# Optimization experiments

Hardware: AMD Instinct MI355X
Metric: run time of the kernel (lower is better)

## Reference

```python
import jax, jax.numpy as jnp
import numpy as np

NBITS = 8          # attn_nbits
GROUP = 32         # per-group size along head_dim for Q/K quantizers
H = 16             # num_heads
EPS = 1e-8


def _ste(x, q):
    # straight-through estimator: forward=q, backward=identity
    return x + jax.lax.stop_gradient(q - x)


def pg_dynamic_quant(x, group_size=GROUP, nbits=NBITS):
    """Per-group symmetric dynamic fake-quant along last dim (ActPGDynamicQuantizer)."""
    qmax = 2.0 ** (nbits - 1) - 1
    lead, D = x.shape[:-1], x.shape[-1]
    xg = x.reshape(*lead, D // group_size, group_size)
    s = jnp.maximum(jnp.max(jnp.abs(xg), axis=-1, keepdims=True) / qmax, EPS)
    q = jnp.clip(jnp.round(xg / s), -qmax - 1.0, qmax) * s
    return _ste(x, q.reshape(x.shape))


def dynamic_quant(x, axis=2, nbits=NBITS):
    """Symmetric dynamic fake-quant, scale shared along `axis` (ActDynamicQuantizer)."""
    qmax = 2.0 ** (nbits - 1) - 1
    s = jnp.maximum(jnp.max(jnp.abs(x), axis=axis, keepdims=True) / qmax, EPS)
    q = jnp.clip(jnp.round(x / s), -qmax - 1.0, qmax) * s
    return _ste(x, q)


def static_scale_quant(x, nbits=NBITS):
    """Unsigned static-scale fake-quant for softmax map in [0,1] (ActStaticScaleQuantizer)."""
    qmax = 2.0 ** nbits - 1
    q = jnp.clip(jnp.round(x * qmax), 0.0, qmax) / qmax
    return _ste(x, q)


def setup_inputs() -> dict:
    key = jax.random.key(0)
    ks = jax.random.split(key, 7)
    B, L, C = 4, 1024, 1024
    return {
        "x":         jax.random.normal(ks[0], (B, L, C), jnp.float32),
        "attn_bias": jax.random.normal(ks[1], (1, 1, L, L), jnp.float32) * 0.1,
        "w_qkv":     jax.random.normal(ks[2], (3 * C, C), jnp.float32) * 0.02,
        "q_bias":    jax.random.normal(ks[3], (C,), jnp.float32) * 0.02,
        "v_bias":    jax.random.normal(ks[4], (C,), jnp.float32) * 0.02,
        "w_proj":    jax.random.normal(ks[5], (C, C), jnp.float32) * 0.02,
        "b_proj":    jax.random.normal(ks[6], (C,), jnp.float32) * 0.02,
    }


def reference(x, attn_bias, w_qkv, q_bias, v_bias, w_proj, b_proj):
    B, L, C = x.shape
    D = C // H
    scale = D ** -0.5
    # qkv projection: bias-free linear + concat(q_bias, zeros_k, v_bias)
    bias = jnp.concatenate([q_bias, jnp.zeros_like(q_bias), v_bias])
    qkv = (x @ w_qkv.T + bias).reshape(B, L, 3, H, D)
    q, k, v = jnp.transpose(qkv, (2, 0, 3, 1, 4))  # each [B,H,L,D]
    # inline fake-quantization (MODE 0 inference path)
    qq = pg_dynamic_quant(q)
    kk = pg_dynamic_quant(k)
    vv = dynamic_quant(v, axis=2)
    attn = jnp.einsum('bhld,bhmd->bhlm', qq * scale, kk) + attn_bias  # [B,H,L,L]
    a = jax.nn.softmax(attn, axis=-1)
    a = static_scale_quant(a)
    out = jnp.einsum('bhlm,bhmd->bhld', a, vv)
    out = jnp.transpose(out, (0, 2, 1, 3)).reshape(B, L, C)
    return out @ w_proj.T + b_proj
```

## Files before the change

### kernel.cpp

```cpp
#include <hip/hip_runtime.h>


typedef unsigned short u16;
typedef unsigned int u32;
typedef __attribute__((ext_vector_type(8))) _Float16 half8;
typedef __attribute__((ext_vector_type(4))) float f32x4;

__device__ __forceinline__ u16 f2b(float f) {
    u32 i;
    __builtin_memcpy(&i, &f, 4);
    return (u16)((i + 0x7FFFu + ((i >> 16) & 1u)) >> 16);
}

__device__ __forceinline__ void split16(float v, u16& hi, u16& lo) {
    _Float16 h = (_Float16)v;
    _Float16 l = (_Float16)(v - (float)h);
    __builtin_memcpy(&hi, &h, 2);
    __builtin_memcpy(&lo, &l, 2);
}

__device__ __forceinline__ int dot4(int a, int b, int c) {
#if __has_builtin(__builtin_amdgcn_sdot4)
    return __builtin_amdgcn_sdot4(a, b, c, false);
#else
    int r = c;
    r += ((a << 24) >> 24) * ((b << 24) >> 24);
    r += ((a << 16) >> 24) * ((b << 16) >> 24);
    r += ((a << 8) >> 24) * ((b << 8) >> 24);
    r += (a >> 24) * (b >> 24);
    return r;
#endif
}

__global__ __launch_bounds__(256) void cvt_bf16w(u16* __restrict__ dst,
                                                 const float* __restrict__ src, int n) {
    int i = (blockIdx.x * 256 + threadIdx.x) * 4;
    if (i + 3 < n) {
        float4 v = *(const float4*)(src + i);
        ushort4 o;
        o.x = f2b(v.x); o.y = f2b(v.y); o.z = f2b(v.z); o.w = f2b(v.w);
        *(ushort4*)(dst + i) = o;
    }
}

__global__ __launch_bounds__(256) void gemm_qkv3(const float* __restrict__ A,
                                                 const float* __restrict__ Bm,
                                                 const float* __restrict__ qbias,
                                                 const float* __restrict__ vbias,
                                                 float* __restrict__ qws,
                                                 float* __restrict__ kws,
                                                 float* __restrict__ vws) {
    __shared__ u16 Ah[128 * 32], Al[128 * 32], Bh[128 * 32], Bl[128 * 32];
    const int t = threadIdx.x;
    const int lane = t & 63, w = t >> 6;
    const int wm = w >> 1, wn = w & 1;
    const int srow = t >> 2, scol = (t & 3) * 8;
    const int lm = lane & 15, lk = (lane >> 4) * 8;
    const int bm = blockIdx.y, bn = blockIdx.x;

    const float* ap = A + (size_t)(bm * 128 + srow) * 1024 + scol;
    const float* bp = Bm + (size_t)(bn * 128 + srow) * 1024 + scol;

    double dacc[4][4][4];
#pragma unroll
    for (int i = 0; i < 4; i++)
#pragma unroll
        for (int j = 0; j < 4; j++)
#pragma unroll
            for (int r = 0; r < 4; r++) dacc[i][j][r] = 0.0;

    for (int slab = 0; slab < 8; slab++) {
        f32x4 acc[4][4];
#pragma unroll
        for (int i = 0; i < 4; i++)
#pragma unroll
            for (int j = 0; j < 4; j++) acc[i][j] = (f32x4){0.f, 0.f, 0.f, 0.f};

        for (int kc = 0; kc < 4; kc++) {
            const int k0 = slab * 128 + kc * 32;
            float vreg[4][8];
#pragma unroll
            for (int e = 0; e < 4; e++) {
                const float* src = (e < 2) ? (ap + (e & 1) * (size_t)64 * 1024 + k0)
                                           : (bp + (e & 1) * (size_t)64 * 1024 + k0);
                float4 v0 = *(const float4*)(src);
                float4 v1 = *(const float4*)(src + 4);
                vreg[e][0] = v0.x; vreg[e][1] = v0.y; vreg[e][2] = v0.z; vreg[e][3] = v0.w;
                vreg[e][4] = v1.x; vreg[e][5] = v1.y; vreg[e][6] = v1.z; vreg[e][7] = v1.w;
            }
            __syncthreads();
#pragma unroll
            for (int e = 0; e < 4; e++) {
                union { u16 us[8]; uint4 v; } ph, pl;
#pragma unroll
                for (int j = 0; j < 8; j++) split16(vreg[e][j], ph.us[j], pl.us[j]);
                u16* dh = (e < 2) ? Ah : Bh;
                u16* dl = (e < 2) ? Al : Bl;
                int row = srow + (e & 1) * 64;
                *(uint4*)(dh + row * 32 + scol) = ph.v;
                *(uint4*)(dl + row * 32 + scol) = pl.v;
            }
            __syncthreads();

            half8 fah[4], fal[4], fbh[4], fbl[4];
#pragma unroll
            for (int i = 0; i < 4; i++) {
                int ra = (wm * 64 + i * 16 + lm) * 32 + lk;
                int rb = (wn * 64 + i * 16 + lm) * 32 + lk;
                fah[i] = *(const half8*)(Ah + ra);
                fal[i] = *(const half8*)(Al + ra);
                fbh[i] = *(const half8*)(Bh + rb);
                fbl[i] = *(const half8*)(Bl + rb);
            }
#pragma unroll
            for (int mi = 0; mi < 4; mi++)
#pragma unroll
                for (int ni = 0; ni < 4; ni++) {
                    acc[mi][ni] = __builtin_amdgcn_mfma_f32_16x16x32_f16(
                        fal[mi], fbh[ni], acc[mi][ni], 0, 0, 0);
                    acc[mi][ni] = __builtin_amdgcn_mfma_f32_16x16x32_f16(
                        fah[mi], fbl[ni], acc[mi][ni], 0, 0, 0);
                    acc[mi][ni] = __builtin_amdgcn_mfma_f32_16x16x32_f16(
                        fah[mi], fbh[ni], acc[mi][ni], 0, 0, 0);
                }
        }
#pragma unroll
        for (int i = 0; i < 4; i++)
#pragma unroll
            for (int j = 0; j < 4; j++)
#pragma unroll
                for (int r = 0; r < 4; r++) dacc[i][j][r] += (double)acc[i][j][r];
    }

    const int rbase = bm * 128 + wm * 64 + (lane >> 4) * 4;
    const int cbase = bn * 128 + wn * 64 + lm;
#pragma unroll
    for (int mi = 0; mi < 4; mi++)
#pragma unroll
        for (int ni = 0; ni < 4; ni++) {
            int col = cbase + ni * 16;
            int sel = col >> 10, cc = col & 1023;
            double bias = (sel == 0) ? (double)qbias[cc]
                        : ((sel == 2) ? (double)vbias[cc] : 0.0);
            float* dst = (sel == 0) ? qws : ((sel == 1) ? kws : vws);
#pragma unroll
            for (int r = 0; r < 4; r++) {
                int row = rbase + mi * 16 + r;
                dst[(size_t)row * 1024 + cc] = (float)(dacc[mi][ni][r] + bias);
            }
        }
}

__global__ __launch_bounds__(256) void quant_qk(const float* __restrict__ pre,
                                                signed char* __restrict__ qout,
                                                double* __restrict__ sout) {
    size_t g = (size_t)blockIdx.x * 256 + threadIdx.x;
    const float* p = pre + g * 32;
    float v[32];
    float amax = 0.f;
#pragma unroll
    for (int i = 0; i < 8; i++) {
        float4 q4 = ((const float4*)p)[i];
        v[i * 4 + 0] = q4.x; v[i * 4 + 1] = q4.y; v[i * 4 + 2] = q4.z; v[i * 4 + 3] = q4.w;
        amax = fmaxf(amax, fmaxf(fmaxf(fabsf(q4.x), fabsf(q4.y)),
                                 fmaxf(fabsf(q4.z), fabsf(q4.w))));
    }
    double s = fmax((double)amax / 127.0, 1e-8);
    sout[g] = s;
    int pk[8];
#pragma unroll
    for (int i = 0; i < 8; i++) {
        int b0 = (int)fmin(fmax(rint((double)v[i * 4 + 0] / s), -128.0), 127.0);
        int b1 = (int)fmin(fmax(rint((double)v[i * 4 + 1] / s), -128.0), 127.0);
        int b2 = (int)fmin(fmax(rint((double)v[i * 4 + 2] / s), -128.0), 127.0);
        int b3 = (int)fmin(fmax(rint((double)v[i * 4 + 3] / s), -128.0), 127.0);
        pk[i] = (b0 & 255) | ((b1 & 255) << 8) | ((b2 & 255) << 16) | ((b3 & 255) << 24);
    }
    int4* d = (int4*)(qout + g * 32);
    d[0] = make_int4(pk[0], pk[1], pk[2], pk[3]);
    d[1] = make_int4(pk[4], pk[5], pk[6], pk[7]);
}

__global__ __launch_bounds__(256) void quant_k(const float* __restrict__ pre,
                                               int* __restrict__ kT,
                                               double* __restrict__ ksT) {
    size_t g = (size_t)blockIdx.x * 256 + threadIdx.x;
    const float* p = pre + g * 32;
    float v[32];
    float amax = 0.f;
#pragma unroll
    for (int i = 0; i < 8; i++) {
        float4 q4 = ((const float4*)p)[i];
        v[i * 4 + 0] = q4.x; v[i * 4 + 1] = q4.y; v[i * 4 + 2] = q4.z; v[i * 4 + 3] = q4.w;
        amax = fmaxf(amax, fmaxf(fmaxf(fabsf(q4.x), fabsf(q4.y)),
                                 fmaxf(fabsf(q4.z), fabsf(q4.w))));
    }
    double s = fmax((double)amax / 127.0, 1e-8);
    int pk[8];
#pragma unroll
    for (int i = 0; i < 8; i++) {
        int b0 = (int)fmin(fmax(rint((double)v[i * 4 + 0] / s), -128.0), 127.0);
        int b1 = (int)fmin(fmax(rint((double)v[i * 4 + 1] / s), -128.0), 127.0);
        int b2 = (int)fmin(fmax(rint((double)v[i * 4 + 2] / s), -128.0), 127.0);
        int b3 = (int)fmin(fmax(rint((double)v[i * 4 + 3] / s), -128.0), 127.0);
        pk[i] = (b0 & 255) | ((b1 & 255) << 8) | ((b2 & 255) << 16) | ((b3 & 255) << 24);
    }
    const int m = (int)((g >> 5) & 1023);
    const int b = (int)(g >> 15);
    const int sub = (int)(g & 31);
    const int h = sub >> 1, pp = sub & 1;
    const int bh = b * 16 + h;
    int* dst = kT + ((size_t)bh * 16 + pp * 8) * 1024 + m;
#pragma unroll
    for (int i = 0; i < 8; i++) dst[i * 1024] = pk[i];
    ksT[((size_t)bh * 2 + pp) * 1024 + m] = s;
}

__global__ __launch_bounds__(256) void vmax_part(const float* __restrict__ vws,
                                                 float* __restrict__ pmax) {
    const int lc = blockIdx.x, b = blockIdx.y, t = threadIdx.x;
#pragma unroll
    for (int j = 0; j < 4; j++) {
        int cc = t + j * 256;
        float mx = 0.f;
        for (int l = 0; l < 64; l++)
            mx = fmaxf(mx, fabsf(vws[((size_t)(b * 1024 + lc * 64 + l)) * 1024 + cc]));
        pmax[(size_t)(b * 16 + lc) * 1024 + cc] = mx;
    }
}

__global__ __launch_bounds__(256) void vmax_final(const float* __restrict__ pmax,
                                                  double* __restrict__ vs) {
    int id = blockIdx.x * 256 + threadIdx.x;
    int b = id >> 10, cc = id & 1023;
    float mx = 0.f;
#pragma unroll
    for (int p = 0; p < 16; p++)
        mx = fmaxf(mx, pmax[(size_t)(b * 16 + p) * 1024 + cc]);
    vs[id] = fmax((double)mx / 127.0, 1e-8);
}

__global__ __launch_bounds__(256) void vquant(float* __restrict__ vws,
                                              const double* __restrict__ vs) {
    size_t e = ((size_t)blockIdx.x * 256 + threadIdx.x) * 4;
    int b = (int)(e >> 20), cc = (int)(e & 1023);
    float4 v = *(const float4*)(vws + e);
    double s0 = vs[b * 1024 + cc], s1 = vs[b * 1024 + cc + 1];
    double s2 = vs[b * 1024 + cc + 2], s3 = vs[b * 1024 + cc + 3];
    float4 o;
    o.x = (float)(fmin(fmax(rint((double)v.x / s0), -128.0), 127.0) * s0);
    o.y = (float)(fmin(fmax(rint((double)v.y / s1), -128.0), 127.0) * s1);
    o.z = (float)(fmin(fmax(rint((double)v.z / s2), -128.0), 127.0) * s2);
    o.w = (float)(fmin(fmax(rint((double)v.w / s3), -128.0), 127.0) * s3);
    *(float4*)(vws + e) = o;
}

__global__ __launch_bounds__(256) void attn(const signed char* __restrict__ qint,
                                            const int* __restrict__ kT,
                                            const double* __restrict__ qs,
                                            const double* __restrict__ ksT,
                                            const float* __restrict__ vfq,
                                            const float* __restrict__ abias,
                                            u16* __restrict__ ctx) {
    __shared__ int    kTs[16][256];
    __shared__ double ks0s[256], ks1s[256];
    __shared__ u32    packed[4][512];
    const int t = threadIdx.x;
    const int wv = t >> 6, lane = t & 63;
    const int qt = blockIdx.x, h = blockIdx.y, b = blockIdx.z;
    const int row = qt * 4 + wv;
    const size_t qrow = (size_t)(b * 1024 + row);
    const int bh = b * 16 + h;

    const int* qv = (const int*)(qint + qrow * 1024 + h * 64);
    int qd[16];
#pragma unroll
    for (int j = 0; j < 4; j++) {
        int4 tmp = ((const int4*)qv)[j];
        qd[j * 4 + 0] = tmp.x; qd[j * 4 + 1] = tmp.y;
        qd[j * 4 + 2] = tmp.z; qd[j * 4 + 3] = tmp.w;
    }
    const double sq0 = qs[qrow * 32 + 2 * h], sq1 = qs[qrow * 32 + 2 * h + 1];
    const int* kTg = kT + (size_t)bh * 16384;
    const double* ks0g = ksT + (size_t)(bh * 2) * 1024;
    const double* ks1g = ksT + (size_t)(bh * 2 + 1) * 1024;
    const float* ab = abias + (size_t)row * 1024;

    double sd[16];
    for (int c = 0; c < 4; c++) {
        if (c) __syncthreads();
#pragma unroll
        for (int r = 0; r < 4; r++) {
            const int j = wv * 4 + r;
            int4 val = *(const int4*)(kTg + (size_t)j * 1024 + c * 256 + 4 * lane);
            *(int4*)(&kTs[j][4 * lane]) = val;
        }
        ks0s[t] = ks0g[c * 256 + t];
        ks1s[t] = ks1g[c * 256 + t];
        __syncthreads();
#pragma unroll
        for (int s = 0; s < 4; s++) {
            const int ml = s * 64 + lane;
            int I0 = 0, I1 = 0;
#pragma unroll
            for (int j = 0; j < 8; j++)  I0 = dot4(qd[j], kTs[j][ml], I0);
#pragma unroll
            for (int j = 8; j < 16; j++) I1 = dot4(qd[j], kTs[j][ml], I1);
            sd[c * 4 + s] = 0.125 * (sq0 * ks0s[ml] * (double)I0
                                   + sq1 * ks1s[ml] * (double)I1)
                          + (double)ab[c * 256 + ml];
        }
    }

    double mx = sd[0];
#pragma unroll
    for (int it = 1; it < 16; it++) mx = fmax(mx, sd[it]);
#pragma unroll
    for (int off = 1; off < 64; off <<= 1) mx = fmax(mx, __shfl_xor(mx, off));
    double sum = 0.0;
#pragma unroll
    for (int it = 0; it < 16; it++) {
        double e = exp(sd[it] - mx);
        sd[it] = e;
        sum += e;
    }
#pragma unroll
    for (int off = 1; off < 64; off <<= 1) sum += __shfl_xor(sum, off);

    int base = 0;
#pragma unroll
    for (int it = 0; it < 16; it++) {
        double a = sd[it] / sum;
        double nd = fmin(fmax(rint(a * 255.0), 0.0), 255.0);
        int ni = (int)nd;
        unsigned long long mk = __ballot(ni != 0);
        if (ni != 0) {
            int pos = base + (int)__popcll(mk & ((1ull << lane) - 1ull));
            packed[wv][pos] = ((u32)ni << 16) | (u32)(it * 64 + lane);
        }
        base += (int)__popcll(mk);
    }
    __syncthreads();

    float acc = 0.f;
    const float* vcol = vfq + ((size_t)b * 1024) * 1024 + h * 64 + lane;
    for (int j = 0; j < base; ++j) {
        u32 p = packed[wv][j];
        float a = (float)(p >> 16) / 255.0f;
        acc = fmaf(a, vcol[(size_t)(p & 1023u) * 1024], acc);
    }
    ctx[qrow * 1024 + h * 64 + lane] = f2b(acc);
}

__global__ __launch_bounds__(256) void gemm_proj(const u16* __restrict__ ctx,
                                                 const u16* __restrict__ wproj,
                                                 const float* __restrict__ bproj,
                                                 float* __restrict__ out) {
    typedef __attribute__((ext_vector_type(8))) short short8;
    __shared__ u16 As[128 * 32], Bs[128 * 32];
    f32x4 acc[4][4];
#pragma unroll
    for (int i = 0; i < 4; i++)
#pragma unroll
        for (int j = 0; j < 4; j++) acc[i][j] = (f32x4){0.f, 0.f, 0.f, 0.f};

    const int t = threadIdx.x;
    const int lane = t & 63, w = t >> 6;
    const int wm = w >> 1, wn = w & 1;
    const int srow = t >> 2, scol = (t & 3) * 8;
    const int lm = lane & 15, lk = (lane >> 4) * 8;
    const int bm = blockIdx.y, bn = blockIdx.x;
    const u16* ap = ctx + (size_t)(bm * 128 + srow) * 1024 + scol;
    const u16* bp = wproj + (size_t)(bn * 128 + srow) * 1024 + scol;

    for (int k0 = 0; k0 < 1024; k0 += 32) {
        uint4 a0 = *(const uint4*)(ap + k0);
        uint4 a1 = *(const uint4*)(ap + (size_t)64 * 1024 + k0);
        uint4 b0 = *(const uint4*)(bp + k0);
        uint4 b1 = *(const uint4*)(bp + (size_t)64 * 1024 + k0);
        __syncthreads();
        *(uint4*)(As + srow * 32 + scol) = a0;
        *(uint4*)(As + (srow + 64) * 32 + scol) = a1;
        *(uint4*)(Bs + srow * 32 + scol) = b0;
        *(uint4*)(Bs + (srow + 64) * 32 + scol) = b1;
        __syncthreads();
        short8 af[4], bfr[4];
#pragma unroll
        for (int i = 0; i < 4; i++) {
            af[i]  = *(const short8*)(As + (wm * 64 + i * 16 + lm) * 32 + lk);
            bfr[i] = *(const short8*)(Bs + (wn * 64 + i * 16 + lm) * 32 + lk);
        }
#pragma unroll
        for (int mi = 0; mi < 4; mi++)
#pragma unroll
            for (int ni = 0; ni < 4; ni++)
                acc[mi][ni] = __builtin_amdgcn_mfma_f32_16x16x32_bf16(
                    af[mi], bfr[ni], acc[mi][ni], 0, 0, 0);
    }

    const int rbase = bm * 128 + wm * 64 + (lane >> 4) * 4;
    const int cbase = bn * 128 + wn * 64 + lm;
#pragma unroll
    for (int mi = 0; mi < 4; mi++)
#pragma unroll
        for (int ni = 0; ni < 4; ni++) {
            int col = cbase + ni * 16;
            float bias = bproj[col];
#pragma unroll
            for (int r = 0; r < 4; r++) {
                int row = rbase + mi * 16 + r;
                out[(size_t)row * 1024 + col] = acc[mi][ni][r] + bias;
            }
        }
}

extern "C" void kernel_launch(void* const* d_in, const int* in_sizes, int n_in,
                              void* d_out, int out_size, void* d_ws, size_t ws_size,
                              hipStream_t stream) {
    const float* x     = (const float*)d_in[0];
    const float* abias = (const float*)d_in[1];
    const float* wqkv  = (const float*)d_in[2];
    const float* qbias = (const float*)d_in[3];
    const float* vbias = (const float*)d_in[4];
    const float* wproj = (const float*)d_in[5];
    const float* bproj = (const float*)d_in[6];
    float* out = (float*)d_out;

    char* ws = (char*)d_ws;
    float*       qpre    = (float*)(ws + 0);
    float*       kpre    = (float*)(ws + 16777216);
    float*       vfq     = (float*)(ws + 33554432);
    u16*         wprojbf = (u16*)  (ws + 50331648);
    signed char* qint    = (signed char*)(ws + 52428800);
    int*         kT      = (int*)  (ws + 56623104);
    double*      qs      = (double*)(ws + 60817408);
    double*      ksT     = (double*)(ws + 61865984);
    double*      vs      = (double*)(ws + 62914560);
    float*       pmax    = (float*)(ws + 62947328);
    u16*         ctx     = (u16*)(ws + 0);

    cvt_bf16w<<<1024, 256, 0, stream>>>(wprojbf, wproj, 1048576);
    gemm_qkv3<<<dim3(24, 32), 256, 0, stream>>>(x, wqkv, qbias, vbias,
                                                qpre, kpre, vfq);
    quant_qk<<<512, 256, 0, stream>>>(qpre, qint, qs);
    quant_k<<<512, 256, 0, stream>>>(kpre, kT, ksT);
    vmax_part<<<dim3(16, 4), 256, 0, stream>>>(vfq, pmax);
    vmax_final<<<16, 256, 0, stream>>>(pmax, vs);
    vquant<<<4096, 256, 0, stream>>>(vfq, vs);
    attn<<<dim3(256, 16, 4), 256, 0, stream>>>(qint, kT, qs, ksT, vfq, abias, ctx);
    gemm_proj<<<dim3(8, 32), 256, 0, stream>>>(ctx, wprojbf, bproj, out);
}
```

Before: 584.1 us.

## Shrink QKV GEMM tile, widen V max reduction, and use custom exp in softmax

The QKV GEMM tile shrinks from 128x128 to 128x64, doubling the grid to 48x32 blocks so more blocks are resident at once. The V column-max partial reduction is split across 64 chunks instead of 16, giving more parallel blocks. The attention softmax replaces the library double exp with a hand-written polynomial exp and turns the per-element division into a multiply by a reciprocal. The smaller tile lowers A/B reuse per block and adds more global reads, and the custom exp and reciprocal can shift rounding slightly before the 8-bit quantization of the softmax output.

```diff
diff --git a/kernel.cpp b/kernel.cpp
--- a/kernel.cpp
+++ b/kernel.cpp
@@ -32,6 +32,29 @@
 #endif
 }
 
+__device__ __forceinline__ double fexp(double x) {
+    double kd = rint(x * 1.4426950408889634);
+    double r = fma(kd, -6.93147180369123816490e-01, x);
+    r = fma(kd, -1.90821492927058770002e-10, r);
+    double p = 2.7557319223985888e-07;
+    p = fma(p, r, 2.7557319223985890e-06);
+    p = fma(p, r, 2.4801587301587302e-05);
+    p = fma(p, r, 1.9841269841269841e-04);
+    p = fma(p, r, 1.3888888888888889e-03);
+    p = fma(p, r, 8.3333333333333333e-03);
+    p = fma(p, r, 4.1666666666666664e-02);
+    p = fma(p, r, 1.6666666666666666e-01);
+    p = fma(p, r, 0.5);
+    p = fma(p, r, 1.0);
+    p = fma(p, r, 1.0);
+    long long bits;
+    __builtin_memcpy(&bits, &p, 8);
+    bits += ((long long)kd) << 52;
+    double e;
+    __builtin_memcpy(&e, &bits, 8);
+    return (x < -700.0) ? 0.0 : e;
+}
+
 __global__ __launch_bounds__(256) void cvt_bf16w(u16* __restrict__ dst,
                                                  const float* __restrict__ src, int n) {
     int i = (blockIdx.x * 256 + threadIdx.x) * 4;
@@ -50,39 +73,38 @@
                                                  float* __restrict__ qws,
                                                  float* __restrict__ kws,
                                                  float* __restrict__ vws) {
-    __shared__ u16 Ah[128 * 32], Al[128 * 32], Bh[128 * 32], Bl[128 * 32];
+    __shared__ u16 Ah[128 * 32], Al[128 * 32], Bh[64 * 32], Bl[64 * 32];
     const int t = threadIdx.x;
     const int lane = t & 63, w = t >> 6;
-    const int wm = w >> 1, wn = w & 1;
     const int srow = t >> 2, scol = (t & 3) * 8;
     const int lm = lane & 15, lk = (lane >> 4) * 8;
     const int bm = blockIdx.y, bn = blockIdx.x;
 
     const float* ap = A + (size_t)(bm * 128 + srow) * 1024 + scol;
-    const float* bp = Bm + (size_t)(bn * 128 + srow) * 1024 + scol;
-
-    double dacc[4][4][4];
-#pragma unroll
-    for (int i = 0; i < 4; i++)
+    const float* bp = Bm + (size_t)(bn * 64 + srow) * 1024 + scol;
+
+    double dacc[2][4][4];
+#pragma unroll
+    for (int i = 0; i < 2; i++)
 #pragma unroll
         for (int j = 0; j < 4; j++)
 #pragma unroll
             for (int r = 0; r < 4; r++) dacc[i][j][r] = 0.0;
 
     for (int slab = 0; slab < 8; slab++) {
-        f32x4 acc[4][4];
-#pragma unroll
-        for (int i = 0; i < 4; i++)
+        f32x4 acc[2][4];
+#pragma unroll
+        for (int i = 0; i < 2; i++)
 #pragma unroll
             for (int j = 0; j < 4; j++) acc[i][j] = (f32x4){0.f, 0.f, 0.f, 0.f};
 
         for (int kc = 0; kc < 4; kc++) {
             const int k0 = slab * 128 + kc * 32;
-            float vreg[4][8];
-#pragma unroll
-            for (int e = 0; e < 4; e++) {
-                const float* src = (e < 2) ? (ap + (e & 1) * (size_t)64 * 1024 + k0)
-                                           : (bp + (e & 1) * (size_t)64 * 1024 + k0);
+            float vreg[3][8];
+#pragma unroll
+            for (int e = 0; e < 3; e++) {
+                const float* src = (e < 2) ? (ap + e * (size_t)64 * 1024 + k0)
+                                           : (bp + k0);
                 float4 v0 = *(const float4*)(src);
                 float4 v1 = *(const float4*)(src + 4);
                 vreg[e][0] = v0.x; vreg[e][1] = v0.y; vreg[e][2] = v0.z; vreg[e][3] = v0.w;
@@ -90,30 +112,33 @@
             }
             __syncthreads();
 #pragma unroll
-            for (int e = 0; e < 4; e++) {
+            for (int e = 0; e < 3; e++) {
                 union { u16 us[8]; uint4 v; } ph, pl;
 #pragma unroll
                 for (int j = 0; j < 8; j++) split16(vreg[e][j], ph.us[j], pl.us[j]);
                 u16* dh = (e < 2) ? Ah : Bh;
                 u16* dl = (e < 2) ? Al : Bl;
-                int row = srow + (e & 1) * 64;
+                int row = (e < 2) ? (srow + e * 64) : srow;
                 *(uint4*)(dh + row * 32 + scol) = ph.v;
                 *(uint4*)(dl + row * 32 + scol) = pl.v;
             }
             __syncthreads();
 
-            half8 fah[4], fal[4], fbh[4], fbl[4];
-#pragma unroll
-            for (int i = 0; i < 4; i++) {
-                int ra = (wm * 64 + i * 16 + lm) * 32 + lk;
-                int rb = (wn * 64 + i * 16 + lm) * 32 + lk;
+            half8 fah[2], fal[2], fbh[4], fbl[4];
+#pragma unroll
+            for (int i = 0; i < 2; i++) {
+                int ra = (w * 32 + i * 16 + lm) * 32 + lk;
                 fah[i] = *(const half8*)(Ah + ra);
                 fal[i] = *(const half8*)(Al + ra);
+            }
+#pragma unroll
+            for (int i = 0; i < 4; i++) {
+                int rb = (i * 16 + lm) * 32 + lk;
                 fbh[i] = *(const half8*)(Bh + rb);
                 fbl[i] = *(const half8*)(Bl + rb);
             }
 #pragma unroll
-            for (int mi = 0; mi < 4; mi++)
+            for (int mi = 0; mi < 2; mi++)
 #pragma unroll
                 for (int ni = 0; ni < 4; ni++) {
                     acc[mi][ni] = __builtin_amdgcn_mfma_f32_16x16x32_f16(
@@ -125,17 +150,17 @@
                 }
         }
 #pragma unroll
-        for (int i = 0; i < 4; i++)
+        for (int i = 0; i < 2; i++)
 #pragma unroll
             for (int j = 0; j < 4; j++)
 #pragma unroll
                 for (int r = 0; r < 4; r++) dacc[i][j][r] += (double)acc[i][j][r];
     }
 
-    const int rbase = bm * 128 + wm * 64 + (lane >> 4) * 4;
-    const int cbase = bn * 128 + wn * 64 + lm;
-#pragma unroll
-    for (int mi = 0; mi < 4; mi++)
+    const int rbase = bm * 128 + w * 32 + (lane >> 4) * 4;
+    const int cbase = bn * 64 + lm;
+#pragma unroll
+    for (int mi = 0; mi < 2; mi++)
 #pragma unroll
         for (int ni = 0; ni < 4; ni++) {
             int col = cbase + ni * 16;
@@ -223,9 +248,9 @@
     for (int j = 0; j < 4; j++) {
         int cc = t + j * 256;
         float mx = 0.f;
-        for (int l = 0; l < 64; l++)
-            mx = fmaxf(mx, fabsf(vws[((size_t)(b * 1024 + lc * 64 + l)) * 1024 + cc]));
-        pmax[(size_t)(b * 16 + lc) * 1024 + cc] = mx;
+        for (int l = 0; l < 16; l++)
+            mx = fmaxf(mx, fabsf(vws[((size_t)(b * 1024 + lc * 16 + l)) * 1024 + cc]));
+        pmax[(size_t)(b * 64 + lc) * 1024 + cc] = mx;
     }
 }
 
@@ -234,9 +259,8 @@
     int id = blockIdx.x * 256 + threadIdx.x;
     int b = id >> 10, cc = id & 1023;
     float mx = 0.f;
-#pragma unroll
-    for (int p = 0; p < 16; p++)
-        mx = fmaxf(mx, pmax[(size_t)(b * 16 + p) * 1024 + cc]);
+    for (int p = 0; p < 64; p++)
+        mx = fmaxf(mx, pmax[(size_t)(b * 64 + p) * 1024 + cc]);
     vs[id] = fmax((double)mx / 127.0, 1e-8);
 }
 
@@ -320,17 +344,18 @@
     double sum = 0.0;
 #pragma unroll
     for (int it = 0; it < 16; it++) {
-        double e = exp(sd[it] - mx);
+        double e = fexp(sd[it] - mx);
         sd[it] = e;
         sum += e;
     }
 #pragma unroll
     for (int off = 1; off < 64; off <<= 1) sum += __shfl_xor(sum, off);
+    const double inv = 1.0 / sum;
 
     int base = 0;
 #pragma unroll
     for (int it = 0; it < 16; it++) {
-        double a = sd[it] / sum;
+        double a = sd[it] * inv;
         double nd = fmin(fmax(rint(a * 255.0), 0.0), 255.0);
         int ni = (int)nd;
         unsigned long long mk = __ballot(ni != 0);
@@ -440,11 +465,11 @@
     u16*         ctx     = (u16*)(ws + 0);
 
     cvt_bf16w<<<1024, 256, 0, stream>>>(wprojbf, wproj, 1048576);
-    gemm_qkv3<<<dim3(24, 32), 256, 0, stream>>>(x, wqkv, qbias, vbias,
+    gemm_qkv3<<<dim3(48, 32), 256, 0, stream>>>(x, wqkv, qbias, vbias,
                                                 qpre, kpre, vfq);
     quant_qk<<<512, 256, 0, stream>>>(qpre, qint, qs);
     quant_k<<<512, 256, 0, stream>>>(kpre, kT, ksT);
-    vmax_part<<<dim3(16, 4), 256, 0, stream>>>(vfq, pmax);
+    vmax_part<<<dim3(64, 4), 256, 0, stream>>>(vfq, pmax);
     vmax_final<<<16, 256, 0, stream>>>(pmax, vs);
     vquant<<<4096, 256, 0, stream>>>(vfq, vs);
     attn<<<dim3(256, 16, 4), 256, 0, stream>>>(qint, kT, qs, ksT, vfq, abias, ctx);
```

Measured after the change: 531.5 us. -9.0%, faster.
